# Kernel optimization log

Hardware: AMD Instinct MI355X
Metric: run time of the kernel (lower is better)

## Reference

```python
import jax, jax.numpy as jnp
import numpy as np
import math

B, T, C, H = 4, 1024, 1024, 16
D = C // H
EPS = 1e-5


def layer_norm(x, w, b):
    mu = jnp.mean(x, axis=-1, keepdims=True)
    var = jnp.mean(jnp.square(x - mu), axis=-1, keepdims=True)
    return (x - mu) * jax.lax.rsqrt(var + EPS) * w + b


def setup_inputs() -> dict:
    key = jax.random.key(0)
    ks = jax.random.split(key, 8)
    s = 0.02
    return {
        "x": jax.random.normal(ks[0], (B, T, C), jnp.float32),
        "attention_mask": jnp.ones((B, T), jnp.float32),
        "ln1_w": jnp.ones((C,), jnp.float32),
        "ln1_b": jnp.zeros((C,), jnp.float32),
        "w_attn": jax.random.normal(ks[1], (C, 3 * C), jnp.float32) * s,
        "b_attn": jnp.zeros((3 * C,), jnp.float32),
        "w_proj": jax.random.normal(ks[2], (C, C), jnp.float32) * s,
        "b_proj": jnp.zeros((C,), jnp.float32),
        "threshold": jnp.float32(0.0005),  # (layer_idx+1)/n_layer * final_token_threshold
        "ln2_w": jnp.ones((C,), jnp.float32),
        "ln2_b": jnp.zeros((C,), jnp.float32),
        "w_fc": jax.random.normal(ks[3], (C, 4 * C), jnp.float32) * s,
        "b_fc": jnp.zeros((4 * C,), jnp.float32),
        "w_fc2": jax.random.normal(ks[4], (4 * C, C), jnp.float32) * s,
        "b_fc2": jnp.zeros((C,), jnp.float32),
    }


def reference(x, attention_mask, ln1_w, ln1_b, w_attn, b_attn, w_proj, b_proj,
              threshold, ln2_w, ln2_b, w_fc, b_fc, w_fc2, b_fc2):
    # ---- attention (eval mode, dropout=0; hard masking_mode) ----
    h = layer_norm(x, ln1_w, ln1_b)
    qkv = h @ w_attn + b_attn                      # (B,T,3C)
    q, k, v = jnp.split(qkv, 3, axis=-1)
    q = q.reshape(B, T, H, D).transpose(0, 2, 1, 3)  # (B,H,T,D)
    k = k.reshape(B, T, H, D).transpose(0, 2, 1, 3)
    v = v.reshape(B, T, H, D).transpose(0, 2, 1, 3)

    scale = 1.0 / math.sqrt(D)
    logits = jnp.einsum("bhqd,bhkd->bhqk", q, k) * scale  # (B,H,T,T)
    causal = jnp.tril(jnp.ones((T, T), bool))
    neg_inf = jnp.float32(-jnp.inf)
    logits = jnp.where(causal[None, None], logits, neg_inf)
    # key-side validity mask (applied in original's manual pass; mask is all-ones
    # here so flash-path y == softmax(causal logits) @ v as well)
    logits = jnp.where(attention_mask[:, None, None, :] == 0, neg_inf, logits)
    att = jax.nn.softmax(logits, axis=-1)

    y = jnp.einsum("bhqk,bhkd->bhqd", att, v)      # (B,H,T,D)
    importance = att.mean(axis=1).mean(axis=1)     # (B,T): mean over heads, then queries

    y = y.transpose(0, 2, 1, 3).reshape(B, T, C)
    x = x + (y @ w_proj + b_proj)

    # ---- hard pruning mask ----
    pruning_mask = (importance >= threshold).astype(x.dtype)
    combined_mask = attention_mask * pruning_mask
    x = x * combined_mask[:, :, None]

    # ---- MLP ----
    h2 = layer_norm(x, ln2_w, ln2_b)
    f = jax.nn.gelu(h2 @ w_fc + b_fc, approximate=False)
    x = x + (f @ w_fc2 + b_fc2)

    pruning_loss = jnp.float32(0.0)  # hard mode -> always 0
    return (x, combined_mask, pruning_loss)
```

## Files before the change

kernel.cpp:

```cpp
#include <hip/hip_runtime.h>
#include <cstdint>
#include <cstring>

typedef unsigned short u16;
typedef short bf16x8 __attribute__((ext_vector_type(8)));
typedef float f32x4 __attribute__((ext_vector_type(4)));

#define MFMA16(a,b,c) __builtin_amdgcn_mfma_f32_16x16x32_bf16(a,b,c,0,0,0)


__device__ __forceinline__ u16 f2bf(float f) {
  union { float f; uint32_t u; } un; un.f = f;
  uint32_t u = un.u;
  u += 0x7FFFu + ((u >> 16) & 1u);
  return (u16)(u >> 16);
}

__device__ __forceinline__ void gl_lds16(const void* g, void* l) {
  __builtin_amdgcn_global_load_lds(
      (__attribute__((address_space(1))) void*)(const_cast<void*>(g)),
      (__attribute__((address_space(3))) void*)l, 16, 0, 0);
}


__global__ __launch_bounds__(256) void transpose_to_bf16(
    const float* __restrict__ W, u16* __restrict__ Wt, int K, int N)
{
  __shared__ float tile[32][33];
  int kt = blockIdx.y * 32, nt = blockIdx.x * 32;
  int tx = threadIdx.x, ty = threadIdx.y;
#pragma unroll
  for (int i = 0; i < 4; ++i)
    tile[ty + i * 8][tx] = W[(size_t)(kt + ty + i * 8) * N + nt + tx];
  __syncthreads();
#pragma unroll
  for (int i = 0; i < 4; ++i)
    Wt[(size_t)(nt + ty + i * 8) * K + kt + tx] = f2bf(tile[tx][ty + i * 8]);
}


__global__ __launch_bounds__(256) void ln_bf16(
    const float* __restrict__ x, const float* __restrict__ wt,
    const float* __restrict__ bs, u16* __restrict__ out)
{
  int row = blockIdx.x;
  int tid = threadIdx.x, lane = tid & 63, w = tid >> 6;
  const float* xr = x + (size_t)row * 1024;
  float4 v = *(const float4*)(xr + tid * 4);
  float s = v.x + v.y + v.z + v.w;
  float sq = v.x * v.x + v.y * v.y + v.z * v.z + v.w * v.w;
#pragma unroll
  for (int o = 1; o < 64; o <<= 1) { s += __shfl_xor(s, o); sq += __shfl_xor(sq, o); }
  __shared__ float ls[4], lq[4];
  if (lane == 0) { ls[w] = s; lq[w] = sq; }
  __syncthreads();
  s = ls[0] + ls[1] + ls[2] + ls[3];
  sq = lq[0] + lq[1] + lq[2] + lq[3];
  float mu = s * (1.f / 1024.f);
  float var = sq * (1.f / 1024.f) - mu * mu;
  float rstd = rsqrtf(var + 1e-5f);
  float4 wv = *(const float4*)(wt + tid * 4);
  float4 bv = *(const float4*)(bs + tid * 4);
  ushort4 o4;
  o4.x = f2bf((v.x - mu) * rstd * wv.x + bv.x);
  o4.y = f2bf((v.y - mu) * rstd * wv.y + bv.y);
  o4.z = f2bf((v.z - mu) * rstd * wv.z + bv.z);
  o4.w = f2bf((v.w - mu) * rstd * wv.w + bv.w);
  *(ushort4*)(out + (size_t)row * 1024 + tid * 4) = o4;
}


__device__ __forceinline__ void gemm_mainloop(
    const u16* __restrict__ A, const u16* __restrict__ Bt,
    int K, int m0, int n0, f32x4 acc[4][4])
{
  __shared__ __align__(16) u16 lA[128 * 32];
  __shared__ __align__(16) u16 lB[128 * 32];

  const int tid = threadIdx.x;
  const int lane = tid & 63;
  const int w = tid >> 6;
  const int wr = (w >> 1) * 64;
  const int wc = (w & 1) * 64;
  const int laneM = lane & 15;
  const int laneK = (lane >> 4) * 8;

#pragma unroll
  for (int i = 0; i < 4; ++i)
#pragma unroll
    for (int j = 0; j < 4; ++j)
      acc[i][j] = f32x4{0.f, 0.f, 0.f, 0.f};

  const int off0 = w * 1024 + lane * 16;
  const int off1 = off0 + 4096;
  const int rA0 = off0 >> 6, cb0 = off0 & 63;
  const int rA1 = off1 >> 6, cb1 = off1 & 63;

  const size_t strideA = (size_t)K * 2;
  const char* gA = (const char*)(A + (size_t)m0 * K);
  const char* gB = (const char*)(Bt + (size_t)n0 * K);
  const char* pA0 = gA + (size_t)rA0 * strideA + cb0;
  const char* pA1 = gA + (size_t)rA1 * strideA + cb1;
  const char* pB0 = gB + (size_t)rA0 * strideA + cb0;
  const char* pB1 = gB + (size_t)rA1 * strideA + cb1;
  char* lA0 = (char*)lA + off0;
  char* lA1 = (char*)lA + off1;
  char* lB0 = (char*)lB + off0;
  char* lB1 = (char*)lB + off1;

  const u16* aRd = lA + (wr + laneM) * 32 + laneK;
  const u16* bRd = lB + (wc + laneM) * 32 + laneK;

  const int nIter = K >> 5;
  for (int it = 0; it < nIter; ++it) {
    gl_lds16(pA0, lA0);
    gl_lds16(pA1, lA1);
    gl_lds16(pB0, lB0);
    gl_lds16(pB1, lB1);
    pA0 += 64; pA1 += 64; pB0 += 64; pB1 += 64;
    __syncthreads();
    bf16x8 af[4], bfr[4];
#pragma unroll
    for (int t = 0; t < 4; ++t) {
      af[t]  = *(const bf16x8*)(aRd + t * 16 * 32);
      bfr[t] = *(const bf16x8*)(bRd + t * 16 * 32);
    }
#pragma unroll
    for (int i = 0; i < 4; ++i)
#pragma unroll
      for (int j = 0; j < 4; ++j)
        acc[i][j] = MFMA16(af[i], bfr[j], acc[i][j]);
    __syncthreads();
  }
}


__global__ __launch_bounds__(256) void gemm_qkv(
    const u16* __restrict__ A, const u16* __restrict__ Bt,
    const float* __restrict__ bias,
    u16* __restrict__ qo, u16* __restrict__ ko, u16* __restrict__ vo)
{
  f32x4 acc[4][4];
  int m0 = blockIdx.y * 128, n0 = blockIdx.x * 128;
  gemm_mainloop(A, Bt, 1024, m0, n0, acc);
  const int lane = threadIdx.x & 63, w = threadIdx.x >> 6;
  const int wr = (w >> 1) * 64, wc = (w & 1) * 64;
  const int laneM = lane & 15, q4 = lane >> 4;
  const int which = (n0 >> 10);
#pragma unroll
  for (int ti = 0; ti < 4; ++ti) {
#pragma unroll
    for (int tj = 0; tj < 4; ++tj) {
      int n = n0 + wc + tj * 16 + laneM;
      int c = n & 1023;
      int hh = c >> 6, d = c & 63;
      float bval = bias[n];
      if (which == 2) {
        int m0r = m0 + wr + ti * 16 + q4 * 4;
        int b = m0r >> 10, t0 = m0r & 1023;
        ushort4 o4;
        o4.x = f2bf(acc[ti][tj][0] + bval);
        o4.y = f2bf(acc[ti][tj][1] + bval);
        o4.z = f2bf(acc[ti][tj][2] + bval);
        o4.w = f2bf(acc[ti][tj][3] + bval);
        *(ushort4*)&vo[((size_t)((b * 16 + hh) * 64 + d)) * 1024 + t0] = o4;
      } else {
        u16* dst = (which == 0) ? qo : ko;
#pragma unroll
        for (int r = 0; r < 4; ++r) {
          int m = m0 + wr + ti * 16 + q4 * 4 + r;
          int b = m >> 10, t = m & 1023;
          dst[((size_t)((b * 16 + hh) * 1024 + t)) * 64 + d] = f2bf(acc[ti][tj][r] + bval);
        }
      }
    }
  }
}

__global__ __launch_bounds__(256) void gemm_proj(
    const u16* __restrict__ A, const u16* __restrict__ Bt,
    const float* __restrict__ bias, const float* __restrict__ xin,
    const float* __restrict__ maskv, float* __restrict__ x2)
{
  f32x4 acc[4][4];
  int m0 = blockIdx.y * 128, n0 = blockIdx.x * 128;
  gemm_mainloop(A, Bt, 1024, m0, n0, acc);
  const int lane = threadIdx.x & 63, w = threadIdx.x >> 6;
  const int wr = (w >> 1) * 64, wc = (w & 1) * 64;
  const int laneM = lane & 15, q4 = lane >> 4;
#pragma unroll
  for (int ti = 0; ti < 4; ++ti) {
#pragma unroll
    for (int tj = 0; tj < 4; ++tj) {
      int n = n0 + wc + tj * 16 + laneM;
      float bval = bias[n];
#pragma unroll
      for (int r = 0; r < 4; ++r) {
        int m = m0 + wr + ti * 16 + q4 * 4 + r;
        float v = xin[(size_t)m * 1024 + n] + acc[ti][tj][r] + bval;
        x2[(size_t)m * 1024 + n] = v * maskv[m];
      }
    }
  }
}

__global__ __launch_bounds__(256) void gemm_fc(
    const u16* __restrict__ A, const u16* __restrict__ Bt,
    const float* __restrict__ bias, u16* __restrict__ fo)
{
  f32x4 acc[4][4];
  int m0 = blockIdx.y * 128, n0 = blockIdx.x * 128;
  gemm_mainloop(A, Bt, 1024, m0, n0, acc);
  const int lane = threadIdx.x & 63, w = threadIdx.x >> 6;
  const int wr = (w >> 1) * 64, wc = (w & 1) * 64;
  const int laneM = lane & 15, q4 = lane >> 4;
#pragma unroll
  for (int ti = 0; ti < 4; ++ti) {
#pragma unroll
    for (int tj = 0; tj < 4; ++tj) {
      int n = n0 + wc + tj * 16 + laneM;
      float bval = bias[n];
#pragma unroll
      for (int r = 0; r < 4; ++r) {
        int m = m0 + wr + ti * 16 + q4 * 4 + r;
        float v = acc[ti][tj][r] + bval;
        float g = 0.5f * v * (1.f + erff(v * 0.70710678118654752f));
        fo[(size_t)m * 4096 + n] = f2bf(g);
      }
    }
  }
}

__global__ __launch_bounds__(256) void gemm_fc2(
    const u16* __restrict__ A, const u16* __restrict__ Bt,
    const float* __restrict__ bias, const float* __restrict__ x2,
    float* __restrict__ xo)
{
  f32x4 acc[4][4];
  int m0 = blockIdx.y * 128, n0 = blockIdx.x * 128;
  gemm_mainloop(A, Bt, 4096, m0, n0, acc);
  const int lane = threadIdx.x & 63, w = threadIdx.x >> 6;
  const int wr = (w >> 1) * 64, wc = (w & 1) * 64;
  const int laneM = lane & 15, q4 = lane >> 4;
#pragma unroll
  for (int ti = 0; ti < 4; ++ti) {
#pragma unroll
    for (int tj = 0; tj < 4; ++tj) {
      int n = n0 + wc + tj * 16 + laneM;
      float bval = bias[n];
#pragma unroll
      for (int r = 0; r < 4; ++r) {
        int m = m0 + wr + ti * 16 + q4 * 4 + r;
        xo[(size_t)m * 1024 + n] = x2[(size_t)m * 1024 + n] + acc[ti][tj][r] + bval;
      }
    }
  }
}


__global__ __launch_bounds__(256) void attn_fwd(
    const u16* __restrict__ qb, const u16* __restrict__ kb, const u16* __restrict__ vtb,
    u16* __restrict__ yb, float* __restrict__ part)
{
  const int bh = blockIdx.x;
  const int qbi = 15 - blockIdx.y;
  const int b = bh >> 4, h = bh & 15;
  const int tid = threadIdx.x, lane = tid & 63, w = tid >> 6;
  const int q0 = qbi * 64;
  const int laneM = lane & 15, q4 = lane >> 4;
  const float scale = 0.125f;

  __shared__ __align__(16) u16 lK[64 * 72];
  __shared__ __align__(16) u16 lV[64 * 72];
  __shared__ __align__(16) u16 lP[4][16 * 72];

  const u16* qrow = qb + ((size_t)(bh * 1024 + q0 + w * 16 + laneM)) * 64 + q4 * 8;
  bf16x8 qf0 = *(const bf16x8*)qrow;
  bf16x8 qf1 = *(const bf16x8*)(qrow + 32);

  const int nkt = qbi + 1;
  const int srow = tid >> 3;
  const int scol = (tid & 7) * 8;
  const u16* kbase = kb + (size_t)bh * 65536;
  const u16* vbase = vtb + (size_t)bh * 65536;

  float lrow[4] = {0.f, 0.f, 0.f, 0.f};
  for (int kt = 0; kt < nkt; ++kt) {
#pragma unroll
    for (int p = 0; p < 2; ++p) {
      int row = srow + p * 32;
      *(uint4*)&lK[row * 72 + scol] =
          *(const uint4*)(kbase + (size_t)(kt * 64 + row) * 64 + scol);
    }
    __syncthreads();
#pragma unroll
    for (int tj = 0; tj < 4; ++tj) {
      const u16* kp = &lK[(tj * 16 + laneM) * 72 + q4 * 8];
      bf16x8 k0 = *(const bf16x8*)kp;
      bf16x8 k1 = *(const bf16x8*)(kp + 32);
      f32x4 z = {0.f, 0.f, 0.f, 0.f};
      z = MFMA16(qf0, k0, z);
      z = MFMA16(qf1, k1, z);
      int kc = kt * 64 + tj * 16 + laneM;
#pragma unroll
      for (int r = 0; r < 4; ++r) {
        int qg = q0 + w * 16 + q4 * 4 + r;
        lrow[r] += (kc <= qg) ? __expf(z[r] * scale) : 0.f;
      }
    }
    __syncthreads();
  }
  float linv[4];
#pragma unroll
  for (int r = 0; r < 4; ++r) {
    float s = lrow[r];
    s += __shfl_xor(s, 1); s += __shfl_xor(s, 2);
    s += __shfl_xor(s, 4); s += __shfl_xor(s, 8);
    linv[r] = 1.f / s;
  }

  f32x4 o_[4];
#pragma unroll
  for (int dt = 0; dt < 4; ++dt) o_[dt] = f32x4{0.f, 0.f, 0.f, 0.f};

  for (int kt = 0; kt < nkt; ++kt) {
#pragma unroll
    for (int p = 0; p < 2; ++p) {
      int row = srow + p * 32;
      *(uint4*)&lK[row * 72 + scol] =
          *(const uint4*)(kbase + (size_t)(kt * 64 + row) * 64 + scol);
      *(uint4*)&lV[row * 72 + scol] =
          *(const uint4*)(vbase + (size_t)row * 1024 + kt * 64 + scol);
    }
    __syncthreads();
    u16* lPw = &lP[w][0];
#pragma unroll
    for (int tj = 0; tj < 4; ++tj) {
      const u16* kp = &lK[(tj * 16 + laneM) * 72 + q4 * 8];
      bf16x8 k0 = *(const bf16x8*)kp;
      bf16x8 k1 = *(const bf16x8*)(kp + 32);
      f32x4 z = {0.f, 0.f, 0.f, 0.f};
      z = MFMA16(qf0, k0, z);
      z = MFMA16(qf1, k1, z);
      int kc = kt * 64 + tj * 16 + laneM;
      float cs = 0.f;
#pragma unroll
      for (int r = 0; r < 4; ++r) {
        int qg = q0 + w * 16 + q4 * 4 + r;
        float pv = (kc <= qg) ? __expf(z[r] * scale) * linv[r] : 0.f;
        cs += pv;
        lPw[(q4 * 4 + r) * 72 + tj * 16 + laneM] = f2bf(pv);
      }
      cs += __shfl_xor(cs, 16);
      cs += __shfl_xor(cs, 32);
      if (lane < 16)
        atomicAdd(&part[(size_t)bh * 1024 + kt * 64 + tj * 16 + lane], cs);
    }
#pragma unroll
    for (int ss = 0; ss < 2; ++ss) {
      bf16x8 pf = *(const bf16x8*)&lP[w][laneM * 72 + ss * 32 + q4 * 8];
#pragma unroll
      for (int dt = 0; dt < 4; ++dt) {
        bf16x8 vf = *(const bf16x8*)&lV[(dt * 16 + laneM) * 72 + ss * 32 + q4 * 8];
        o_[dt] = MFMA16(pf, vf, o_[dt]);
      }
    }
    __syncthreads();
  }

#pragma unroll
  for (int dt = 0; dt < 4; ++dt)
#pragma unroll
    for (int r = 0; r < 4; ++r) {
      int qg = q0 + w * 16 + q4 * 4 + r;
      yb[((size_t)(b * 1024 + qg)) * 1024 + h * 64 + dt * 16 + laneM] = f2bf(o_[dt][r]);
    }
}


__global__ __launch_bounds__(256) void finalize_mask(
    const float* __restrict__ part, const float* __restrict__ amask,
    const float* __restrict__ thr, float* __restrict__ mask_ws,
    float* __restrict__ out_mask, float* __restrict__ out_loss)
{
  int i = blockIdx.x * 256 + threadIdx.x;
  if (i >= 4096) return;
  int b = i >> 10;
  int t = i & 1023;
  float s = 0.f;
#pragma unroll
  for (int hh = 0; hh < 16; ++hh) s += part[(size_t)(b * 16 + hh) * 1024 + t];
  float imp = s * (1.0f / 16384.0f);
  float mv = (imp >= thr[0]) ? amask[i] : 0.f;
  mask_ws[i] = mv;
  out_mask[i] = mv;
  if (i == 0) out_loss[0] = 0.f;
}


extern "C" void kernel_launch(void* const* d_in, const int* in_sizes, int n_in,
                              void* d_out, int out_size, void* d_ws, size_t ws_size,
                              hipStream_t stream) {
  const float* x      = (const float*)d_in[0];
  const float* amask  = (const float*)d_in[1];
  const float* ln1w   = (const float*)d_in[2];
  const float* ln1b   = (const float*)d_in[3];
  const float* w_attn = (const float*)d_in[4];
  const float* b_attn = (const float*)d_in[5];
  const float* w_proj = (const float*)d_in[6];
  const float* b_proj = (const float*)d_in[7];
  const float* thr    = (const float*)d_in[8];
  const float* ln2w   = (const float*)d_in[9];
  const float* ln2b   = (const float*)d_in[10];
  const float* w_fc   = (const float*)d_in[11];
  const float* b_fc   = (const float*)d_in[12];
  const float* w_fc2  = (const float*)d_in[13];
  const float* b_fc2  = (const float*)d_in[14];
  float* out = (float*)d_out;

  char* ws = (char*)d_ws;
  size_t off = 0;
  auto alloc = [&](size_t bytes) -> char* {
    char* p = ws + off;
    off += (bytes + 255) & ~(size_t)255;
    return p;
  };
  u16* wattnT = (u16*)alloc((size_t)3072 * 1024 * 2);
  u16* wprojT = (u16*)alloc((size_t)1024 * 1024 * 2);
  u16* wfcT   = (u16*)alloc((size_t)4096 * 1024 * 2);
  u16* wfc2T  = (u16*)alloc((size_t)1024 * 4096 * 2);
  u16* hbuf   = (u16*)alloc((size_t)4096 * 1024 * 2);
  u16* qbuf   = (u16*)alloc((size_t)64 * 1024 * 64 * 2);
  u16* kbuf   = (u16*)alloc((size_t)64 * 1024 * 64 * 2);
  u16* vtbuf  = (u16*)alloc((size_t)64 * 64 * 1024 * 2);
  u16* ybuf   = (u16*)alloc((size_t)4096 * 1024 * 2);
  float* part = (float*)alloc((size_t)64 * 1024 * 4);
  float* maskws = (float*)alloc((size_t)4096 * 4);
  float* x2   = (float*)alloc((size_t)4096 * 1024 * 4);
  u16* h2     = (u16*)alloc((size_t)4096 * 1024 * 2);
  u16* fbuf   = (u16*)alloc((size_t)4096 * 4096 * 2);

  dim3 tb(32, 8);
  transpose_to_bf16<<<dim3(96, 32),  tb, 0, stream>>>(w_attn, wattnT, 1024, 3072);
  transpose_to_bf16<<<dim3(32, 32),  tb, 0, stream>>>(w_proj, wprojT, 1024, 1024);
  transpose_to_bf16<<<dim3(128, 32), tb, 0, stream>>>(w_fc,   wfcT,   1024, 4096);
  transpose_to_bf16<<<dim3(32, 128), tb, 0, stream>>>(w_fc2,  wfc2T,  4096, 1024);

  hipMemsetAsync(part, 0, (size_t)64 * 1024 * 4, stream);

  ln_bf16<<<4096, 256, 0, stream>>>(x, ln1w, ln1b, hbuf);

  gemm_qkv<<<dim3(24, 32), 256, 0, stream>>>(hbuf, wattnT, b_attn, qbuf, kbuf, vtbuf);

  attn_fwd<<<dim3(64, 16), 256, 0, stream>>>(qbuf, kbuf, vtbuf, ybuf, part);

  finalize_mask<<<16, 256, 0, stream>>>(part, amask, thr, maskws,
                                        out + 4194304, out + 4198400);

  gemm_proj<<<dim3(8, 32), 256, 0, stream>>>(ybuf, wprojT, b_proj, x, maskws, x2);

  ln_bf16<<<4096, 256, 0, stream>>>(x2, ln2w, ln2b, h2);

  gemm_fc<<<dim3(32, 32), 256, 0, stream>>>(h2, wfcT, b_fc, fbuf);

  gemm_fc2<<<dim3(8, 32), 256, 0, stream>>>(fbuf, wfc2T, b_fc2, x2, out);
}
```

Measured before the change: 418.5 us.

## Double-buffer GEMM LDS tiles and split-K the fc2 GEMM with atomics

The shared GEMM mainloop now uses two LDS buffers, so the global-to-LDS load of the next K-slice is issued before the MFMAs on the current slice, and one barrier per iteration is removed. The fc2 GEMM (K=4096, only 256 blocks) is split into 4 K-chunks for 1024 blocks, which accumulate into the output with float atomicAdd after a prefill kernel writes the residual plus bias. This targets load latency and low occupancy in fc2, at the cost of twice the LDS, an extra elementwise pass, atomic traffic, and non-deterministic summation order.

```diff
diff --git a/kernel.cpp b/kernel.cpp
--- a/kernel.cpp
+++ b/kernel.cpp
@@ -70,12 +70,12 @@
 }
 
 
-__device__ __forceinline__ void gemm_mainloop(
-    const u16* __restrict__ A, const u16* __restrict__ Bt,
-    int K, int m0, int n0, f32x4 acc[4][4])
-{
-  __shared__ __align__(16) u16 lA[128 * 32];
-  __shared__ __align__(16) u16 lB[128 * 32];
+__device__ __forceinline__ void gemm_mainloop_db(
+    const u16* __restrict__ Abase, const u16* __restrict__ Bbase,
+    int lda, int ldb, int nIter, f32x4 acc[4][4])
+{
+  __shared__ __align__(16) u16 lA[2][128 * 32];
+  __shared__ __align__(16) u16 lB[2][128 * 32];
 
   const int tid = threadIdx.x;
   const int lane = tid & 63;
@@ -96,29 +96,34 @@
   const int rA0 = off0 >> 6, cb0 = off0 & 63;
   const int rA1 = off1 >> 6, cb1 = off1 & 63;
 
-  const size_t strideA = (size_t)K * 2;
-  const char* gA = (const char*)(A + (size_t)m0 * K);
-  const char* gB = (const char*)(Bt + (size_t)n0 * K);
-  const char* pA0 = gA + (size_t)rA0 * strideA + cb0;
-  const char* pA1 = gA + (size_t)rA1 * strideA + cb1;
-  const char* pB0 = gB + (size_t)rA0 * strideA + cb0;
-  const char* pB1 = gB + (size_t)rA1 * strideA + cb1;
-  char* lA0 = (char*)lA + off0;
-  char* lA1 = (char*)lA + off1;
-  char* lB0 = (char*)lB + off0;
-  char* lB1 = (char*)lB + off1;
-
-  const u16* aRd = lA + (wr + laneM) * 32 + laneK;
-  const u16* bRd = lB + (wc + laneM) * 32 + laneK;
-
-  const int nIter = K >> 5;
+  const size_t sA = (size_t)lda * 2;
+  const size_t sB = (size_t)ldb * 2;
+  const char* pA0 = (const char*)Abase + (size_t)rA0 * sA + cb0;
+  const char* pA1 = (const char*)Abase + (size_t)rA1 * sA + cb1;
+  const char* pB0 = (const char*)Bbase + (size_t)rA0 * sB + cb0;
+  const char* pB1 = (const char*)Bbase + (size_t)rA1 * sB + cb1;
+  char* dA0 = (char*)&lA[0][0] + off0;
+  char* dA1 = (char*)&lA[0][0] + off1;
+  char* dB0 = (char*)&lB[0][0] + off0;
+  char* dB1 = (char*)&lB[0][0] + off1;
+
+  gl_lds16(pA0, dA0); gl_lds16(pA1, dA1);
+  gl_lds16(pB0, dB0); gl_lds16(pB1, dB1);
+  pA0 += 64; pA1 += 64; pB0 += 64; pB1 += 64;
+  __syncthreads();
+
   for (int it = 0; it < nIter; ++it) {
-    gl_lds16(pA0, lA0);
-    gl_lds16(pA1, lA1);
-    gl_lds16(pB0, lB0);
-    gl_lds16(pB1, lB1);
-    pA0 += 64; pA1 += 64; pB0 += 64; pB1 += 64;
-    __syncthreads();
+    const int cur = it & 1;
+    const int nb = cur ^ 1;
+    if (it + 1 < nIter) {
+      gl_lds16(pA0, dA0 + nb * 8192);
+      gl_lds16(pA1, dA1 + nb * 8192);
+      gl_lds16(pB0, dB0 + nb * 8192);
+      gl_lds16(pB1, dB1 + nb * 8192);
+      pA0 += 64; pA1 += 64; pB0 += 64; pB1 += 64;
+    }
+    const u16* aRd = &lA[cur][(wr + laneM) * 32 + laneK];
+    const u16* bRd = &lB[cur][(wc + laneM) * 32 + laneK];
     bf16x8 af[4], bfr[4];
 #pragma unroll
     for (int t = 0; t < 4; ++t) {
@@ -130,7 +135,7 @@
 #pragma unroll
       for (int j = 0; j < 4; ++j)
         acc[i][j] = MFMA16(af[i], bfr[j], acc[i][j]);
-    __syncthreads();
+    if (it + 1 < nIter) __syncthreads();
   }
 }
 
@@ -142,7 +147,7 @@
 {
   f32x4 acc[4][4];
   int m0 = blockIdx.y * 128, n0 = blockIdx.x * 128;
-  gemm_mainloop(A, Bt, 1024, m0, n0, acc);
+  gemm_mainloop_db(A + (size_t)m0 * 1024, Bt + (size_t)n0 * 1024, 1024, 1024, 32, acc);
   const int lane = threadIdx.x & 63, w = threadIdx.x >> 6;
   const int wr = (w >> 1) * 64, wc = (w & 1) * 64;
   const int laneM = lane & 15, q4 = lane >> 4;
@@ -184,7 +189,7 @@
 {
   f32x4 acc[4][4];
   int m0 = blockIdx.y * 128, n0 = blockIdx.x * 128;
-  gemm_mainloop(A, Bt, 1024, m0, n0, acc);
+  gemm_mainloop_db(A + (size_t)m0 * 1024, Bt + (size_t)n0 * 1024, 1024, 1024, 32, acc);
   const int lane = threadIdx.x & 63, w = threadIdx.x >> 6;
   const int wr = (w >> 1) * 64, wc = (w & 1) * 64;
   const int laneM = lane & 15, q4 = lane >> 4;
@@ -210,7 +215,7 @@
 {
   f32x4 acc[4][4];
   int m0 = blockIdx.y * 128, n0 = blockIdx.x * 128;
-  gemm_mainloop(A, Bt, 1024, m0, n0, acc);
+  gemm_mainloop_db(A + (size_t)m0 * 1024, Bt + (size_t)n0 * 1024, 1024, 1024, 32, acc);
   const int lane = threadIdx.x & 63, w = threadIdx.x >> 6;
   const int wr = (w >> 1) * 64, wc = (w & 1) * 64;
   const int laneM = lane & 15, q4 = lane >> 4;
@@ -231,14 +236,26 @@
   }
 }
 
-__global__ __launch_bounds__(256) void gemm_fc2(
+__global__ __launch_bounds__(256) void prefill_out(
+    const float* __restrict__ x2, const float* __restrict__ bias,
+    float* __restrict__ out)
+{
+  int i = blockIdx.x * 256 + threadIdx.x;
+  int col4 = i & 255;
+  float4 v = ((const float4*)x2)[i];
+  float4 b = ((const float4*)bias)[col4];
+  float4 o; o.x = v.x + b.x; o.y = v.y + b.y; o.z = v.z + b.z; o.w = v.w + b.w;
+  ((float4*)out)[i] = o;
+}
+
+__global__ __launch_bounds__(256) void gemm_fc2_splitk(
     const u16* __restrict__ A, const u16* __restrict__ Bt,
-    const float* __restrict__ bias, const float* __restrict__ x2,
-    float* __restrict__ xo)
+    float* __restrict__ out)
 {
   f32x4 acc[4][4];
-  int m0 = blockIdx.y * 128, n0 = blockIdx.x * 128;
-  gemm_mainloop(A, Bt, 4096, m0, n0, acc);
+  int m0 = blockIdx.y * 128, n0 = blockIdx.x * 128, k0 = blockIdx.z * 1024;
+  gemm_mainloop_db(A + (size_t)m0 * 4096 + k0, Bt + (size_t)n0 * 4096 + k0,
+                   4096, 4096, 32, acc);
   const int lane = threadIdx.x & 63, w = threadIdx.x >> 6;
   const int wr = (w >> 1) * 64, wc = (w & 1) * 64;
   const int laneM = lane & 15, q4 = lane >> 4;
@@ -247,11 +264,10 @@
 #pragma unroll
     for (int tj = 0; tj < 4; ++tj) {
       int n = n0 + wc + tj * 16 + laneM;
-      float bval = bias[n];
 #pragma unroll
       for (int r = 0; r < 4; ++r) {
         int m = m0 + wr + ti * 16 + q4 * 4 + r;
-        xo[(size_t)m * 1024 + n] = x2[(size_t)m * 1024 + n] + acc[ti][tj][r] + bval;
+        atomicAdd(&out[(size_t)m * 1024 + n], acc[ti][tj][r]);
       }
     }
   }
@@ -463,5 +479,7 @@
 
   gemm_fc<<<dim3(32, 32), 256, 0, stream>>>(h2, wfcT, b_fc, fbuf);
 
-  gemm_fc2<<<dim3(8, 32), 256, 0, stream>>>(fbuf, wfc2T, b_fc2, x2, out);
-}
+  prefill_out<<<4096, 256, 0, stream>>>(x2, b_fc2, out);
+
+  gemm_fc2_splitk<<<dim3(8, 32, 4), 256, 0, stream>>>(fbuf, wfc2T, out);
+}
```

Measured after the change: 419.1 us. No clear change (+0.1%).
